# Optimization experiments

Hardware: AMD Instinct MI355X
Metric: run time of the kernel (lower is better)

The kernel has to match this reference:

```python
import jax, jax.numpy as jnp
import numpy as np

C_REG = 50.0  # soft-SVM regularization from __init__ default C=50


def kronecker(A, B):
    # torch: einsum('ab,cd->acbd').view(a*c, b*d)
    return jnp.einsum('ab,cd->acbd', A, B).reshape(
        A.shape[0] * B.shape[0], A.shape[1] * B.shape[1])


def setup_inputs() -> dict:
    key = jax.random.key(0)
    k1, k2, k3, k4 = jax.random.split(key, 4)
    N_c, N_S, N_Q, C, W, H = 16, 25, 15, 3, 32, 32
    D_feat = 640
    S_k = jax.random.normal(k1, (N_c, N_S, C, W, H), dtype=jnp.float32)
    Q_k = jax.random.normal(k2, (N_c, N_Q, C, W, H), dtype=jnp.float32)
    # base_net modeled as Flatten -> Linear(C*W*H, D_feat), no bias
    W_base = jax.random.normal(k3, (C * W * H, D_feat), dtype=jnp.float32) * 0.02
    gamma = jax.random.normal(k4, (1,), dtype=jnp.float32)
    return {"S_k": S_k, "Q_k": Q_k, "W_base": W_base, "gamma": gamma}


def reference(S_k, Q_k, W_base, gamma):
    N_c, N_S = S_k.shape[:2]
    N_Q = Q_k.shape[1]
    # base_net: flatten image dims, project to features
    f_x = S_k.reshape(N_c * N_S, -1) @ W_base  # placeholder
    f_x = Q_k.reshape(N_c * N_Q, -1) @ W_base          # [N_c*N_Q, D]
    K = S_k.reshape(N_c * N_S, -1) @ W_base            # [N_c*N_S, D]
    # kernel matrix + ridge
    aul = K @ K.T + C_REG * jnp.eye(N_c * N_S, dtype=K.dtype)  # [N_c*N_S, N_c*N_S]
    # explicit Kronecker expansion to the full (N_c^2*N_S) system
    Q = kronecker(jnp.eye(N_c, dtype=K.dtype), aul)    # [N_c^2*N_S, N_c^2*N_S]
    p = kronecker(jnp.eye(N_c, dtype=K.dtype),
                  jnp.ones((1, N_S), dtype=K.dtype)).reshape(-1, 1)
    alpha = jnp.linalg.solve(Q, jax.lax.stop_gradient(p))  # p is detached in torch
    alpha = alpha.reshape(N_c, -1)                     # [N_c, N_c*N_S]
    w_k = alpha @ K                                    # [N_c, D]
    logits = -gamma * (f_x @ w_k.T)                    # [N_c*N_Q, N_c]
    return logits
```

## Files before the change

### kernel.cpp

```cpp
#include <hip/hip_runtime.h>
#include <math.h>

#define DIN 3072
#define DF 640
#define MROWS 400
#define QROWS 240
#define NMAT 400
#define PN 416
#define NRHS 16
#define CREG 50.0f
#define PVSTEPS 5
#define CSTEPS 25
#define KSPLIT 4
#define GBLK 13
#define SCOLS 32
#define SPAD 40
#define FPAD 72
#define MTILES 28

typedef __attribute__((ext_vector_type(8))) short bf8v;
typedef __attribute__((ext_vector_type(4))) short s4v;
typedef __attribute__((ext_vector_type(4))) float f32x4;

__device__ __forceinline__ short bf16_rn(float x) {
  unsigned u = __float_as_uint(x);
  u += 0x7FFFu + ((u >> 16) & 1u);
  return (short)(u >> 16);
}
__device__ __forceinline__ void split_sh(float x, short& h, short& l) {
  h = bf16_rn(x);
  float hf = __uint_as_float(((unsigned)(unsigned short)h) << 16);
  l = bf16_rn(x - hf);
}
__device__ __forceinline__ float bf2f(short h) {
  return __uint_as_float(((unsigned)(unsigned short)h) << 16);
}

__global__ __launch_bounds__(256) void gemm_feat_sk(const float* __restrict__ S,
                                                    const float* __restrict__ Qm,
                                                    const float* __restrict__ Wb,
                                                    float* __restrict__ Acc) {
  __shared__ short Ash[64][FPAD];
  __shared__ short Asl[64][FPAD];
  __shared__ short Bsh[64][FPAD];
  __shared__ short Bsl[64][FPAD];
  int tid = threadIdx.x;
  int wave = tid >> 6, lane = tid & 63, l16 = lane & 15, quad = lane >> 4;
  int by = blockIdx.y, bx = blockIdx.x, bz = blockIdx.z;
  int colBase = bx * 64;
  int kbeg = bz * (DIN / KSPLIT), kend = kbeg + (DIN / KSPLIT);
  f32x4 acc[4] = {{0,0,0,0},{0,0,0,0},{0,0,0,0},{0,0,0,0}};
  for (int k0 = kbeg; k0 < kend; k0 += 64) {
    __syncthreads();
#pragma unroll
    for (int p = 0; p < 4; ++p) {
      int cid = tid + 256 * p;
      int row = cid >> 4, kc4 = (cid & 15) * 4;
      int arow = by * 64 + row;
      const float* sr = (arow < MROWS) ? (S + (size_t)arow * DIN)
                                       : (Qm + (size_t)(arow - MROWS) * DIN);
      float4 v = *reinterpret_cast<const float4*>(sr + k0 + kc4);
      s4v hv, lv;
      short h, l;
      split_sh(v.x, h, l); hv[0] = h; lv[0] = l;
      split_sh(v.y, h, l); hv[1] = h; lv[1] = l;
      split_sh(v.z, h, l); hv[2] = h; lv[2] = l;
      split_sh(v.w, h, l); hv[3] = h; lv[3] = l;
      *reinterpret_cast<s4v*>(&Ash[row][kc4]) = hv;
      *reinterpret_cast<s4v*>(&Asl[row][kc4]) = lv;
    }
#pragma unroll
    for (int p = 0; p < 4; ++p) {
      int cid = tid + 256 * p;
      int r = cid >> 4, c4 = (cid & 15) * 4;
      float4 w = *reinterpret_cast<const float4*>(Wb + (size_t)(k0 + r) * DF + colBase + c4);
      short h, l;
      split_sh(w.x, h, l); Bsh[c4 + 0][r] = h; Bsl[c4 + 0][r] = l;
      split_sh(w.y, h, l); Bsh[c4 + 1][r] = h; Bsl[c4 + 1][r] = l;
      split_sh(w.z, h, l); Bsh[c4 + 2][r] = h; Bsl[c4 + 2][r] = l;
      split_sh(w.w, h, l); Bsh[c4 + 3][r] = h; Bsl[c4 + 3][r] = l;
    }
    __syncthreads();
#pragma unroll
    for (int kk = 0; kk < 64; kk += 32) {
      int ko = kk + quad * 8;
      bf8v ah = *reinterpret_cast<const bf8v*>(&Ash[wave * 16 + l16][ko]);
      bf8v al = *reinterpret_cast<const bf8v*>(&Asl[wave * 16 + l16][ko]);
#pragma unroll
      for (int t = 0; t < 4; ++t) {
        bf8v bh = *reinterpret_cast<const bf8v*>(&Bsh[t * 16 + l16][ko]);
        bf8v bl = *reinterpret_cast<const bf8v*>(&Bsl[t * 16 + l16][ko]);
        acc[t] = __builtin_amdgcn_mfma_f32_16x16x32_bf16(ah, bh, acc[t], 0, 0, 0);
        acc[t] = __builtin_amdgcn_mfma_f32_16x16x32_bf16(ah, bl, acc[t], 0, 0, 0);
        acc[t] = __builtin_amdgcn_mfma_f32_16x16x32_bf16(al, bh, acc[t], 0, 0, 0);
      }
    }
  }
  float* Ap = Acc + (size_t)bz * 640 * DF;
  int row0 = by * 64 + wave * 16;
#pragma unroll
  for (int t = 0; t < 4; ++t)
#pragma unroll
    for (int r = 0; r < 4; ++r) {
      int row = row0 + quad * 4 + r;
      int col = colBase + t * 16 + l16;
      Ap[(size_t)row * DF + col] = acc[t][r];
    }
}

__global__ __launch_bounds__(256) void feat_reduce(const float* __restrict__ Acc,
                                                   short* __restrict__ Kh,
                                                   short* __restrict__ Kl,
                                                   float* __restrict__ FX,
                                                   float* __restrict__ zbuf) {
  int tid = threadIdx.x;
  if (blockIdx.x == 0) {
    for (int e = tid; e < 14160; e += 256) zbuf[e] = 0.f;
  }
  int idx = blockIdx.x * 256 + tid;
  if (idx >= 640 * DF) return;
  float v = Acc[idx] + Acc[idx + 409600] + Acc[idx + 819200] + Acc[idx + 1228800];
  int row = idx / DF, col = idx - row * DF;
  if (row < MROWS) {
    short h, l; split_sh(v, h, l);
    Kh[(size_t)row * DF + col] = h;
    Kl[(size_t)row * DF + col] = l;
  } else {
    FX[(size_t)(row - MROWS) * DF + col] = v;
  }
}

__global__ __launch_bounds__(256) void gemm_aul(const short* __restrict__ Kh,
                                                const short* __restrict__ Kl,
                                                short* __restrict__ Aph,
                                                short* __restrict__ Apl) {
  int tid = threadIdx.x;
  int wave = tid >> 6, lane = tid & 63;
  int l16 = lane & 15, quad = lane >> 4;
  int row0 = blockIdx.y * 64 + wave * 16;
  int colBase = blockIdx.x * 64;
  bool aValid = (row0 < MROWS);
  const bf8v bzero = {0,0,0,0,0,0,0,0};
  f32x4 acc[4] = {{0,0,0,0},{0,0,0,0},{0,0,0,0},{0,0,0,0}};
  for (int k0 = 0; k0 < DF; k0 += 32) {
    int ka = k0 + quad * 8;
    bf8v ah = bzero, al = bzero;
    if (aValid) {
      size_t ao = (size_t)(row0 + l16) * DF + ka;
      ah = *reinterpret_cast<const bf8v*>(Kh + ao);
      al = *reinterpret_cast<const bf8v*>(Kl + ao);
    }
#pragma unroll
    for (int t = 0; t < 4; ++t) {
      int colt = colBase + t * 16;
      bf8v bh = bzero, bl = bzero;
      if (colt < MROWS) {
        size_t bo = (size_t)(colt + l16) * DF + ka;
        bh = *reinterpret_cast<const bf8v*>(Kh + bo);
        bl = *reinterpret_cast<const bf8v*>(Kl + bo);
      }
      acc[t] = __builtin_amdgcn_mfma_f32_16x16x32_bf16(ah, bh, acc[t], 0, 0, 0);
      acc[t] = __builtin_amdgcn_mfma_f32_16x16x32_bf16(ah, bl, acc[t], 0, 0, 0);
      acc[t] = __builtin_amdgcn_mfma_f32_16x16x32_bf16(al, bh, acc[t], 0, 0, 0);
    }
  }
  if (row0 >= PN) return;
#pragma unroll
  for (int t = 0; t < 4; ++t) {
    int colt = colBase + t * 16;
    if (colt >= PN) continue;
#pragma unroll
    for (int r = 0; r < 4; ++r) {
      int row = row0 + quad * 4 + r;
      int col = colt + l16;
      float v = acc[t][r];
      if (row == col && row < MROWS) v += CREG;
      short h, l; split_sh(v, h, l);
      size_t o = (size_t)row * PN + col;
      Aph[o] = h; Apl[o] = l;
    }
  }
}

__global__ __launch_bounds__(256) void solve_and_m(const short* __restrict__ Aph,
                                                   const short* __restrict__ Apl,
                                                   const float* __restrict__ FX,
                                                   const short* __restrict__ Kh,
                                                   const short* __restrict__ Kl,
                                                   float* __restrict__ Y0,
                                                   float* __restrict__ Y1,
                                                   float* __restrict__ V0,
                                                   float* __restrict__ V1,
                                                   float* __restrict__ rq,
                                                   unsigned* __restrict__ bar,
                                                   float* __restrict__ X,
                                                   float* __restrict__ M) {
  int tid = threadIdx.x, b = blockIdx.x;
  int wave = tid >> 6, lane = tid & 63, l16 = lane & 15, quad = lane >> 4;
  const bf8v bzero = {0,0,0,0,0,0,0,0};

  if (b >= GBLK) {
    int mt = b - GBLK;
    int mb = mt / 7, nb = mt - (mt / 7) * 7;
    int q0 = mb * 64 + wave * 16;
    f32x4 acc[4] = {{0,0,0,0},{0,0,0,0},{0,0,0,0},{0,0,0,0}};
    int arow = q0 + l16;
    bool aOk = (arow < QROWS);
    const float* fr = FX + (size_t)(aOk ? arow : 0) * DF;
    for (int k0 = 0; k0 < DF; k0 += 32) {
      int ka = k0 + quad * 8;
      bf8v ah = bzero, al = bzero;
      if (aOk) {
        float4 a0 = *reinterpret_cast<const float4*>(fr + ka);
        float4 a1 = *reinterpret_cast<const float4*>(fr + ka + 4);
        float av[8] = {a0.x, a0.y, a0.z, a0.w, a1.x, a1.y, a1.z, a1.w};
#pragma unroll
        for (int j = 0; j < 8; ++j) { short h, l; split_sh(av[j], h, l); ah[j] = h; al[j] = l; }
      }
#pragma unroll
      for (int t = 0; t < 4; ++t) {
        int n = nb * 64 + t * 16 + l16;
        bf8v bh = bzero, bl = bzero;
        if (n < NMAT) {
          bh = *reinterpret_cast<const bf8v*>(Kh + (size_t)n * DF + ka);
          bl = *reinterpret_cast<const bf8v*>(Kl + (size_t)n * DF + ka);
        }
        acc[t] = __builtin_amdgcn_mfma_f32_16x16x32_bf16(ah, bh, acc[t], 0, 0, 0);
        acc[t] = __builtin_amdgcn_mfma_f32_16x16x32_bf16(ah, bl, acc[t], 0, 0, 0);
        acc[t] = __builtin_amdgcn_mfma_f32_16x16x32_bf16(al, bh, acc[t], 0, 0, 0);
      }
    }
#pragma unroll
    for (int t = 0; t < 4; ++t)
#pragma unroll
      for (int r = 0; r < 4; ++r) {
        int row = q0 + quad * 4 + r;
        int col = nb * 64 + t * 16 + l16;
        if (row < QROWS && col < NMAT) M[(size_t)row * NMAT + col] = acc[t][r];
      }
    return;
  }

  __shared__ short AsT_h[PN][SPAD];
  __shared__ short AsT_l[PN][SPAD];
  __shared__ short dbT_h[16][SPAD];
  __shared__ short dbT_l[16][SPAD];
  __shared__ float pvp[SCOLS], pvc[SCOLS];
  __shared__ float scal[2];
  int r0 = b * SCOLS;

  for (int e = tid; e < SCOLS * (PN / 8); e += 256) {
    int jl = e / (PN / 8), ic = e - (e / (PN / 8)) * (PN / 8);
    bf8v vh = *reinterpret_cast<const bf8v*>(Aph + (size_t)(r0 + jl) * PN + ic * 8);
    bf8v vl = *reinterpret_cast<const bf8v*>(Apl + (size_t)(r0 + jl) * PN + ic * 8);
#pragma unroll
    for (int u = 0; u < 8; ++u) {
      AsT_h[ic * 8 + u][jl] = vh[u];
      AsT_l[ic * 8 + u][jl] = vl[u];
    }
  }
  for (int e = tid; e < 16 * SPAD; e += 256) {
    (&dbT_h[0][0])[e] = 0; (&dbT_l[0][0])[e] = 0;
  }
  __syncthreads();
  if (tid < SCOLS) {
    int gi = r0 + tid;
    float v = (gi < NMAT) ? (1.f + 0.125f * (float)(gi & 7)) : 0.f;
    pvc[tid] = v; pvp[tid] = 0.f;
    dbT_h[0][tid] = bf16_rn(v);
  }
  __syncthreads();

  unsigned ph = 0;
  auto gridbar = [&]() {
    __syncthreads();
    ++ph;
    if (tid == 0) {
      unsigned tgt = ph * GBLK;
      __hip_atomic_fetch_add(bar, 1u, __ATOMIC_RELEASE, __HIP_MEMORY_SCOPE_AGENT);
      while (__hip_atomic_load(bar, __ATOMIC_RELAXED, __HIP_MEMORY_SCOPE_AGENT) < tgt)
        __builtin_amdgcn_s_sleep(2);
    }
    __syncthreads();
  };

  for (int s = 0; s < PVSTEPS; ++s) {
    float* Yv = (s & 1) ? V1 : V0;
    for (int t = wave; t < 26; t += 4) {
      f32x4 acc = {0, 0, 0, 0};
      bf8v bh = *reinterpret_cast<const bf8v*>(&dbT_h[l16][quad * 8]);
      bf8v ah = *reinterpret_cast<const bf8v*>(&AsT_h[t * 16 + l16][quad * 8]);
      acc = __builtin_amdgcn_mfma_f32_16x16x32_bf16(ah, bh, acc, 0, 0, 0);
      if (l16 == 0) {
#pragma unroll
        for (int r_ = 0; r_ < 4; ++r_)
          atomicAdd(&Yv[t * 16 + quad * 4 + r_], acc[r_]);
      }
    }
    gridbar();
    if (tid < SCOLS) {
      float y = atomicExch(&Yv[r0 + tid], 0.f);
      float v = y * (1.f / 4096.f);
      pvp[tid] = pvc[tid];
      pvc[tid] = v;
      dbT_h[0][tid] = bf16_rn(v);
    }
    __syncthreads();
  }
  if (tid == 0) {
    float n = 0.f, dd = 0.f;
    for (int u = 0; u < SCOLS; ++u) { n += pvp[u] * pvc[u]; dd += pvp[u] * pvp[u]; }
    atomicAdd(&rq[0], n);
    atomicAdd(&rq[1], dd);
  }
  gridbar();
  if (tid == 0) {
    float rn = atomicAdd(&rq[0], 0.f), rd = atomicAdd(&rq[1], 0.f);
    float rqv = 4096.f * rn / rd;
    float bb = 1.3f * rqv;
    if (!(bb > 800.f)) bb = 12000.f;
    if (bb > 100000.f) bb = 100000.f;
    scal[0] = 0.5f * (bb + CREG);
    scal[1] = 0.5f * (bb - CREG);
  }
  __syncthreads();
  float theta = scal[0], delta = scal[1];
  float sigma = theta / delta, rho = 1.f / sigma;

  float xr[2], rr[2], dr[2];
#pragma unroll
  for (int m = 0; m < 2; ++m) {
    int rl = (tid >> 4) + 16 * m, c = tid & 15, gi = r0 + rl;
    float pc = (gi < NMAT && (gi / 25) == c) ? 1.f : 0.f;
    xr[m] = 0.f; rr[m] = pc; dr[m] = pc / theta;
    short h, l; split_sh(dr[m], h, l);
    dbT_h[c][rl] = h; dbT_l[c][rl] = l;
  }
  __syncthreads();

  for (int k = 0; k < CSTEPS - 1; ++k) {
    float* Yv = (k & 1) ? Y1 : Y0;
    for (int t = wave; t < 26; t += 4) {
      f32x4 acc = {0, 0, 0, 0};
      bf8v bh = *reinterpret_cast<const bf8v*>(&dbT_h[l16][quad * 8]);
      bf8v bl = *reinterpret_cast<const bf8v*>(&dbT_l[l16][quad * 8]);
      bf8v ah = *reinterpret_cast<const bf8v*>(&AsT_h[t * 16 + l16][quad * 8]);
      bf8v al = *reinterpret_cast<const bf8v*>(&AsT_l[t * 16 + l16][quad * 8]);
      acc = __builtin_amdgcn_mfma_f32_16x16x32_bf16(ah, bh, acc, 0, 0, 0);
      acc = __builtin_amdgcn_mfma_f32_16x16x32_bf16(ah, bl, acc, 0, 0, 0);
      acc = __builtin_amdgcn_mfma_f32_16x16x32_bf16(al, bh, acc, 0, 0, 0);
#pragma unroll
      for (int r_ = 0; r_ < 4; ++r_)
        atomicAdd(&Yv[(t * 16 + quad * 4 + r_) * 16 + l16], acc[r_]);
    }
    gridbar();
    float rho1 = 1.f / (2.f * sigma - rho);
    float s1 = rho1 * rho, s2 = 2.f * rho1 / delta;
    rho = rho1;
#pragma unroll
    for (int m = 0; m < 2; ++m) {
      int rl = (tid >> 4) + 16 * m, c = tid & 15, gi = r0 + rl;
      float mv = atomicExch(&Yv[gi * 16 + c], 0.f);
      xr[m] += dr[m];
      rr[m] -= mv;
      float dn = s1 * dr[m] + s2 * rr[m];
      dr[m] = dn;
      short h, l; split_sh(dn, h, l);
      dbT_h[c][rl] = h; dbT_l[c][rl] = l;
    }
    __syncthreads();
  }
#pragma unroll
  for (int m = 0; m < 2; ++m) {
    int rl = (tid >> 4) + 16 * m, c = tid & 15, gi = r0 + rl;
    if (gi < NMAT) X[gi * NRHS + c] = xr[m] + dr[m];
  }
}

__global__ __launch_bounds__(256) void logits_kernel(const float* __restrict__ M,
                                                     const float* __restrict__ X,
                                                     const float* __restrict__ gamma,
                                                     float* __restrict__ out) {
  __shared__ float Xs[NMAT * NRHS];
  __shared__ float Ms[16][NMAT];
  int tid = threadIdx.x;
  int q0 = blockIdx.x * 16;
  for (int e = tid; e < NMAT * NRHS; e += 256) Xs[e] = X[e];
  for (int e = tid; e < 16 * NMAT; e += 256) {
    int rl = e / NMAT, i = e - (e / NMAT) * NMAT;
    Ms[rl][i] = M[(size_t)(q0 + rl) * NMAT + i];
  }
  __syncthreads();
  int ql = tid >> 4, c = tid & 15;
  float acc = 0.f;
  for (int i = 0; i < NMAT; ++i) acc += Ms[ql][i] * Xs[i * NRHS + c];
  out[(size_t)(q0 + ql) * NRHS + c] = -gamma[0] * acc;
}

extern "C" void kernel_launch(void* const* d_in, const int* in_sizes, int n_in,
                              void* d_out, int out_size, void* d_ws, size_t ws_size,
                              hipStream_t stream) {
  const float* S = (const float*)d_in[0];
  const float* Qm = (const float*)d_in[1];
  const float* Wb = (const float*)d_in[2];
  const float* gamma = (const float*)d_in[3];
  float* out = (float*)d_out;
  char* base = (char*)d_ws;
  short* Kh   = (short*)(base);
  short* Kl   = (short*)(base + 512000);
  float* FX   = (float*)(base + 1024000);
  short* Aph  = (short*)(base + 1638400);
  short* Apl  = (short*)(base + 1984512);
  float* Mm   = (float*)(base + 2330624);
  float* Xb   = (float*)(base + 2714624);
  unsigned* bar = (unsigned*)(base + 2740224);
  float* rq   = (float*)(base + 2740232);
  float* zbuf = (float*)(base + 2740224);
  float* Y0   = (float*)(base + 2740288);
  float* Y1   = (float*)(base + 2766912);
  float* V0   = (float*)(base + 2793536);
  float* V1   = (float*)(base + 2795200);
  float* Acc  = (float*)(base + 2796864);

  gemm_feat_sk<<<dim3(10, 10, KSPLIT), 256, 0, stream>>>(S, Qm, Wb, Acc);
  feat_reduce<<<1600, 256, 0, stream>>>(Acc, Kh, Kl, FX, zbuf);
  gemm_aul<<<dim3(7, 7), 256, 0, stream>>>(Kh, Kl, Aph, Apl);
  solve_and_m<<<GBLK + MTILES, 256, 0, stream>>>(Aph, Apl, FX, Kh, Kl,
                                                 Y0, Y1, V0, V1, rq, bar, Xb, Mm);
  logits_kernel<<<15, 256, 0, stream>>>(Mm, Xb, gamma, out);
}
```

Measured before the change: 245.5 us.

## Prefetch feature GEMM tiles into registers and fuse logits into solver kernel

```diff
diff --git a/kernel.cpp b/kernel.cpp
--- a/kernel.cpp
+++ b/kernel.cpp
@@ -49,38 +49,51 @@
   int by = blockIdx.y, bx = blockIdx.x, bz = blockIdx.z;
   int colBase = bx * 64;
   int kbeg = bz * (DIN / KSPLIT), kend = kbeg + (DIN / KSPLIT);
-  f32x4 acc[4] = {{0,0,0,0},{0,0,0,0},{0,0,0,0},{0,0,0,0}};
-  for (int k0 = kbeg; k0 < kend; k0 += 64) {
-    __syncthreads();
+  int arow = by * 64 + (tid >> 4);
+  const float* sr = (arow < MROWS) ? (S + (size_t)arow * DIN)
+                                   : (Qm + (size_t)(arow - MROWS) * DIN);
+  int kc4 = (tid & 15) * 4;
+  float4 ar4[4], br4[4];
+  auto load_regs = [&](int kk) {
 #pragma unroll
     for (int p = 0; p < 4; ++p) {
-      int cid = tid + 256 * p;
-      int row = cid >> 4, kc4 = (cid & 15) * 4;
-      int arow = by * 64 + row;
-      const float* sr = (arow < MROWS) ? (S + (size_t)arow * DIN)
-                                       : (Qm + (size_t)(arow - MROWS) * DIN);
-      float4 v = *reinterpret_cast<const float4*>(sr + k0 + kc4);
-      s4v hv, lv;
-      short h, l;
-      split_sh(v.x, h, l); hv[0] = h; lv[0] = l;
-      split_sh(v.y, h, l); hv[1] = h; lv[1] = l;
-      split_sh(v.z, h, l); hv[2] = h; lv[2] = l;
-      split_sh(v.w, h, l); hv[3] = h; lv[3] = l;
+      int rowoff = 16 * p;
+      const float* srp;
+      {
+        int ar_ = by * 64 + (tid >> 4) + rowoff;
+        srp = (ar_ < MROWS) ? (S + (size_t)ar_ * DIN) : (Qm + (size_t)(ar_ - MROWS) * DIN);
+      }
+      ar4[p] = *reinterpret_cast<const float4*>(srp + kk + kc4);
+      int r = (tid >> 4) + rowoff;
+      br4[p] = *reinterpret_cast<const float4*>(Wb + (size_t)(kk + r) * DF + colBase + kc4);
+    }
+  };
+  auto split_write = [&]() {
+#pragma unroll
+    for (int p = 0; p < 4; ++p) {
+      int row = (tid >> 4) + 16 * p;
+      s4v hv, lv; short h, l;
+      split_sh(ar4[p].x, h, l); hv[0] = h; lv[0] = l;
+      split_sh(ar4[p].y, h, l); hv[1] = h; lv[1] = l;
+      split_sh(ar4[p].z, h, l); hv[2] = h; lv[2] = l;
+      split_sh(ar4[p].w, h, l); hv[3] = h; lv[3] = l;
       *reinterpret_cast<s4v*>(&Ash[row][kc4]) = hv;
       *reinterpret_cast<s4v*>(&Asl[row][kc4]) = lv;
-    }
-#pragma unroll
-    for (int p = 0; p < 4; ++p) {
-      int cid = tid + 256 * p;
-      int r = cid >> 4, c4 = (cid & 15) * 4;
-      float4 w = *reinterpret_cast<const float4*>(Wb + (size_t)(k0 + r) * DF + colBase + c4);
-      short h, l;
-      split_sh(w.x, h, l); Bsh[c4 + 0][r] = h; Bsl[c4 + 0][r] = l;
-      split_sh(w.y, h, l); Bsh[c4 + 1][r] = h; Bsl[c4 + 1][r] = l;
-      split_sh(w.z, h, l); Bsh[c4 + 2][r] = h; Bsl[c4 + 2][r] = l;
-      split_sh(w.w, h, l); Bsh[c4 + 3][r] = h; Bsl[c4 + 3][r] = l;
-    }
-    __syncthreads();
+      split_sh(br4[p].x, h, l); Bsh[kc4 + 0][row] = h; Bsl[kc4 + 0][row] = l;
+      split_sh(br4[p].y, h, l); Bsh[kc4 + 1][row] = h; Bsl[kc4 + 1][row] = l;
+      split_sh(br4[p].z, h, l); Bsh[kc4 + 2][row] = h; Bsl[kc4 + 2][row] = l;
+      split_sh(br4[p].w, h, l); Bsh[kc4 + 3][row] = h; Bsl[kc4 + 3][row] = l;
+    }
+  };
+  f32x4 acc[4] = {{0,0,0,0},{0,0,0,0},{0,0,0,0},{0,0,0,0}};
+  load_regs(kbeg);
+  split_write();
+  __syncthreads();
+  int k0 = kbeg;
+  while (true) {
+    int kn = k0 + 64;
+    bool more = (kn < kend);
+    if (more) load_regs(kn);
 #pragma unroll
     for (int kk = 0; kk < 64; kk += 32) {
       int ko = kk + quad * 8;
@@ -95,6 +108,11 @@
         acc[t] = __builtin_amdgcn_mfma_f32_16x16x32_bf16(al, bh, acc[t], 0, 0, 0);
       }
     }
+    if (!more) break;
+    __syncthreads();
+    split_write();
+    __syncthreads();
+    k0 = kn;
   }
   float* Ap = Acc + (size_t)bz * 640 * DF;
   int row0 = by * 64 + wave * 16;
@@ -112,10 +130,13 @@
                                                    short* __restrict__ Kh,
                                                    short* __restrict__ Kl,
                                                    float* __restrict__ FX,
-                                                   float* __restrict__ zbuf) {
+                                                   float* __restrict__ zbuf,
+                                                   float* __restrict__ out) {
   int tid = threadIdx.x;
   if (blockIdx.x == 0) {
     for (int e = tid; e < 14160; e += 256) zbuf[e] = 0.f;
+  } else if (blockIdx.x == 1) {
+    for (int e = tid; e < QROWS * NRHS; e += 256) out[e] = 0.f;
   }
   int idx = blockIdx.x * 256 + tid;
   if (idx >= 640 * DF) return;
@@ -187,14 +208,16 @@
                                                    const float* __restrict__ FX,
                                                    const short* __restrict__ Kh,
                                                    const short* __restrict__ Kl,
+                                                   const float* __restrict__ gamma,
                                                    float* __restrict__ Y0,
                                                    float* __restrict__ Y1,
                                                    float* __restrict__ V0,
                                                    float* __restrict__ V1,
                                                    float* __restrict__ rq,
                                                    unsigned* __restrict__ bar,
-                                                   float* __restrict__ X,
-                                                   float* __restrict__ M) {
+                                                   unsigned* __restrict__ mflag,
+                                                   float* __restrict__ M,
+                                                   float* __restrict__ out) {
   int tid = threadIdx.x, b = blockIdx.x;
   int wave = tid >> 6, lane = tid & 63, l16 = lane & 15, quad = lane >> 4;
   const bf8v bzero = {0,0,0,0,0,0,0,0};
@@ -236,17 +259,23 @@
       for (int r = 0; r < 4; ++r) {
         int row = q0 + quad * 4 + r;
         int col = nb * 64 + t * 16 + l16;
-        if (row < QROWS && col < NMAT) M[(size_t)row * NMAT + col] = acc[t][r];
-      }
+        if (row < QROWS && col < NMAT)
+          __hip_atomic_store(&M[(size_t)row * NMAT + col], acc[t][r],
+                             __ATOMIC_RELAXED, __HIP_MEMORY_SCOPE_AGENT);
+      }
+    __syncthreads();
+    if (tid == 0)
+      __hip_atomic_fetch_add(mflag, 1u, __ATOMIC_RELEASE, __HIP_MEMORY_SCOPE_AGENT);
     return;
   }
 
-  __shared__ short AsT_h[PN][SPAD];
+  __shared__ __align__(16) short AsT_h[PN][SPAD];
   __shared__ short AsT_l[PN][SPAD];
   __shared__ short dbT_h[16][SPAD];
   __shared__ short dbT_l[16][SPAD];
   __shared__ float pvp[SCOLS], pvc[SCOLS];
   __shared__ float scal[2];
+  __shared__ float XsL[SCOLS][NRHS + 1];
   int r0 = b * SCOLS;
 
   for (int e = tid; e < SCOLS * (PN / 8); e += 256) {
@@ -372,29 +401,33 @@
   }
 #pragma unroll
   for (int m = 0; m < 2; ++m) {
-    int rl = (tid >> 4) + 16 * m, c = tid & 15, gi = r0 + rl;
-    if (gi < NMAT) X[gi * NRHS + c] = xr[m] + dr[m];
-  }
-}
-
-__global__ __launch_bounds__(256) void logits_kernel(const float* __restrict__ M,
-                                                     const float* __restrict__ X,
-                                                     const float* __restrict__ gamma,
-                                                     float* __restrict__ out) {
-  __shared__ float Xs[NMAT * NRHS];
-  __shared__ float Ms[16][NMAT];
-  int tid = threadIdx.x;
-  int q0 = blockIdx.x * 16;
-  for (int e = tid; e < NMAT * NRHS; e += 256) Xs[e] = X[e];
-  for (int e = tid; e < 16 * NMAT; e += 256) {
-    int rl = e / NMAT, i = e - (e / NMAT) * NMAT;
-    Ms[rl][i] = M[(size_t)(q0 + rl) * NMAT + i];
-  }
-  __syncthreads();
-  int ql = tid >> 4, c = tid & 15;
-  float acc = 0.f;
-  for (int i = 0; i < NMAT; ++i) acc += Ms[ql][i] * Xs[i * NRHS + c];
-  out[(size_t)(q0 + ql) * NRHS + c] = -gamma[0] * acc;
+    int rl = (tid >> 4) + 16 * m, c = tid & 15;
+    XsL[rl][c] = xr[m] + dr[m];
+  }
+  __syncthreads();
+  if (tid == 0) {
+    while (__hip_atomic_load(mflag, __ATOMIC_RELAXED, __HIP_MEMORY_SCOPE_AGENT) < MTILES)
+      __builtin_amdgcn_s_sleep(2);
+  }
+  __syncthreads();
+  float* Msl = reinterpret_cast<float*>(&AsT_h[0][0]);
+  for (int e = tid; e < QROWS * SCOLS; e += 256) {
+    int q = e >> 5, i = e & 31;
+    float v = 0.f;
+    if (r0 + i < NMAT)
+      v = __hip_atomic_load(&M[(size_t)q * NMAT + r0 + i],
+                            __ATOMIC_RELAXED, __HIP_MEMORY_SCOPE_AGENT);
+    Msl[e] = v;
+  }
+  __syncthreads();
+  float g = -gamma[0];
+  int c = tid & 15;
+  for (int q = tid >> 4; q < QROWS; q += 16) {
+    float s = 0.f;
+#pragma unroll
+    for (int i = 0; i < SCOLS; ++i) s += Msl[q * SCOLS + i] * XsL[i][c];
+    atomicAdd(&out[q * NRHS + c], g * s);
+  }
 }
 
 extern "C" void kernel_launch(void* const* d_in, const int* in_sizes, int n_in,
@@ -412,9 +445,9 @@
   short* Aph  = (short*)(base + 1638400);
   short* Apl  = (short*)(base + 1984512);
   float* Mm   = (float*)(base + 2330624);
-  float* Xb   = (float*)(base + 2714624);
   unsigned* bar = (unsigned*)(base + 2740224);
   float* rq   = (float*)(base + 2740232);
+  unsigned* mflag = (unsigned*)(base + 2740240);
   float* zbuf = (float*)(base + 2740224);
   float* Y0   = (float*)(base + 2740288);
   float* Y1   = (float*)(base + 2766912);
@@ -423,9 +456,9 @@
   float* Acc  = (float*)(base + 2796864);
 
   gemm_feat_sk<<<dim3(10, 10, KSPLIT), 256, 0, stream>>>(S, Qm, Wb, Acc);
-  feat_reduce<<<1600, 256, 0, stream>>>(Acc, Kh, Kl, FX, zbuf);
+  feat_reduce<<<1600, 256, 0, stream>>>(Acc, Kh, Kl, FX, zbuf, out);
   gemm_aul<<<dim3(7, 7), 256, 0, stream>>>(Kh, Kl, Aph, Apl);
-  solve_and_m<<<GBLK + MTILES, 256, 0, stream>>>(Aph, Apl, FX, Kh, Kl,
-                                                 Y0, Y1, V0, V1, rq, bar, Xb, Mm);
-  logits_kernel<<<15, 256, 0, stream>>>(Mm, Xb, gamma, out);
-}
+  solve_and_m<<<GBLK + MTILES, 256, 0, stream>>>(Aph, Apl, FX, Kh, Kl, gamma,
+                                                 Y0, Y1, V0, V1, rq, bar, mflag,
+                                                 Mm, out);
+}
```

Result: faster. 229.2 us (-6.6%).
